# Optimization experiments

Measured on AMD Instinct MI355X. Metric: run time of the kernel, lower is better.

The kernel has to match this reference:

```python
import jax, jax.numpy as jnp
import numpy as np

B, QL, D = 4, 1024, 1024
H, HD = 16, 64
KVL = 2048


def setup_inputs() -> dict:
    key = jax.random.key(0)
    ks = jax.random.split(key, 6)
    scale = 1.0 / np.sqrt(D)
    return {
        "hidden_states": jax.random.normal(ks[0], (B, QL, D), dtype=jnp.float32),
        "key_states": jax.random.normal(ks[1], (B, H, KVL, HD), dtype=jnp.float32),
        "value_states": jax.random.normal(ks[2], (B, H, KVL, HD), dtype=jnp.float32),
        "attention_mask": jnp.zeros((B, 1, 1, KVL), dtype=jnp.float32),
        "Wq": jax.random.normal(ks[3], (D, D), dtype=jnp.float32) * scale,
        "Wo": jax.random.normal(ks[4], (D, D), dtype=jnp.float32) * scale,
    }


def reference(hidden_states, key_states, value_states, attention_mask, Wq, Wo):
    batch = hidden_states.shape[0]
    # Q projection (T5 Linear has no bias), split heads: [B, H, Q, HD]
    q = jnp.einsum("bqd,de->bqe", hidden_states, Wq)
    q = q.reshape(batch, -1, H, HD).transpose(0, 2, 1, 3)
    # NOTE: T5 attention has NO 1/sqrt(d) scaling
    scores = jnp.einsum("bhqd,bhkd->bhqk", q, key_states) + attention_mask
    attn = jax.nn.softmax(scores.astype(jnp.float32), axis=-1).astype(scores.dtype)
    out = jnp.einsum("bhqk,bhkd->bhqd", attn, value_states)
    out = out.transpose(0, 2, 1, 3).reshape(batch, -1, H * HD)
    return jnp.einsum("bqe,ed->bqd", out, Wo)
```

## Files before the change

kernel.cpp:

```cpp
#include <hip/hip_runtime.h>
#include <hip/hip_bf16.h>
#include <hip/hip_fp16.h>
#include <stdint.h>

typedef _Float16 f16;
typedef _Float16 f16x2 __attribute__((ext_vector_type(2)));
typedef _Float16 f16x4 __attribute__((ext_vector_type(4)));
typedef _Float16 f16x8 __attribute__((ext_vector_type(8)));
typedef float f32x4 __attribute__((ext_vector_type(4)));
typedef float f32x16 __attribute__((ext_vector_type(16)));

#define B_ 4
#define QL_ 1024
#define D_ 1024
#define H_ 16
#define HD_ 64
#define KVL_ 2048
#define L2E 1.44269504088896f

__device__ __forceinline__ void g2lds16(const void* g, void* l) {
    __builtin_amdgcn_global_load_lds(
        (const __attribute__((address_space(1))) uint32_t*)g,
        (__attribute__((address_space(3))) uint32_t*)l,
        16, 0, 0);
}

union U8 { uint32_t u[4]; f16x8 v; };

__device__ __forceinline__ uint32_t pkrtz(float a, float b) {
    auto t = __builtin_amdgcn_cvt_pkrtz(a, b);
    return __builtin_bit_cast(uint32_t, t);
}

__global__ void preprocess_slim(const float* __restrict__ hs, f16* __restrict__ hs_h,
                                const float* __restrict__ Wq, f16* __restrict__ Wq_t) {
    __shared__ float t[64][65];
    int bid = blockIdx.x, tid = threadIdx.x;
    if (bid < 1024) {
        const int n4 = (B_ * QL_ * D_) / 4;
        for (int i = bid * 256 + tid; i < n4; i += 1024 * 256) {
            float4 v = ((const float4*)hs)[i];
            f16x4 o = { (f16)v.x, (f16)v.y, (f16)v.z, (f16)v.w };
            ((f16x4*)hs_h)[i] = o;
        }
    } else {
        int b2 = bid - 1024;
        int k0 = (b2 >> 4) << 6, n0 = (b2 & 15) << 6;
        int rr = tid >> 4, c4 = (tid & 15) << 2;
#pragma unroll
        for (int i = 0; i < 4; ++i) {
            int r = i * 16 + rr;
            float4 v = *(const float4*)(Wq + (size_t)(k0 + r) * 1024 + n0 + c4);
            t[r][c4 + 0] = v.x; t[r][c4 + 1] = v.y; t[r][c4 + 2] = v.z; t[r][c4 + 3] = v.w;
        }
        __syncthreads();
#pragma unroll
        for (int i = 0; i < 4; ++i) {
            int n = i * 16 + rr;
            f16x4 o;
#pragma unroll
            for (int j = 0; j < 4; ++j) o[j] = (f16)t[c4 + j][n];
            *(f16x4*)(Wq_t + (size_t)(n0 + n) * 1024 + k0 + c4) = o;
        }
    }
}

__global__ __launch_bounds__(512) void gemm0_fused(
    const f16* __restrict__ A, const f16* __restrict__ BT, f16* __restrict__ q_h,
    const float* __restrict__ K, f16* __restrict__ K_h,
    const float* __restrict__ V, f16* __restrict__ V_t,
    const float* __restrict__ Wo, f16* __restrict__ Wo_t,
    const float* __restrict__ mask, float* __restrict__ mL) {
    __shared__ char shmem[49152];
    int bid = blockIdx.x, tid = threadIdx.x;

    if (bid < 512) {
        char* Alds = shmem;
        char* Blds = shmem + 32768;
        int xcd = bid & 7, sx = bid >> 3;
        int bm = xcd * 4 + (sx & 3);
        int bn = sx >> 2;
        int w = tid >> 6, l = tid & 63;
        int l15 = l & 15, lg = l >> 4;
        int wm = w >> 1, wn = w & 1;
        f32x4 acc[2][2] = {};

        const char* ag0; const char* ag1; int ao0, ao1;
        {
            int i0 = w, i1 = w + 8;
            int r0 = i0 * 8 + (l >> 3), r1 = i1 * 8 + (l >> 3);
            int c0 = (l & 7) ^ (r0 & 7), c1 = (l & 7) ^ (r1 & 7);
            ag0 = (const char*)A + ((size_t)(bm * 128 + r0) * 1024 + c0 * 8) * 2;
            ag1 = (const char*)A + ((size_t)(bm * 128 + r1) * 1024 + c1 * 8) * 2;
            ao0 = i0 * 1024; ao1 = i1 * 1024;
        }
        int rB = w * 8 + (l >> 3);
        int ccB = (l & 7) ^ (rB & 7);
        const char* bgp = (const char*)BT + ((size_t)(bn * 64 + rB) * 1024 + ccB * 8) * 2;
        int boB = w * 1024;

        int aoff[2][2], boff[2][2];
#pragma unroll
        for (int ks = 0; ks < 2; ++ks)
#pragma unroll
            for (int m = 0; m < 2; ++m) {
                int ra = wm * 32 + m * 16 + l15;
                aoff[ks][m] = ra * 128 + ((ks * 64 + lg * 16) ^ ((ra & 7) << 4));
                int rb = wn * 32 + m * 16 + l15;
                boff[ks][m] = rb * 128 + ((ks * 64 + lg * 16) ^ ((rb & 7) << 4));
            }

#define GSTAGE(buf, soff)                                          \
    {                                                              \
        g2lds16(ag0 + (soff), Alds + (buf) * 16384 + ao0);         \
        g2lds16(ag1 + (soff), Alds + (buf) * 16384 + ao1);         \
        g2lds16(bgp + (soff), Blds + (buf) * 8192 + boB);          \
    }
#define GCOMP(buf)                                                               \
    _Pragma("unroll") for (int ks = 0; ks < 2; ++ks) {                           \
        f16x8 af[2], bf[2];                                                      \
        af[0] = *(const f16x8*)(Alds + (buf) * 16384 + aoff[ks][0]);             \
        af[1] = *(const f16x8*)(Alds + (buf) * 16384 + aoff[ks][1]);             \
        bf[0] = *(const f16x8*)(Blds + (buf) * 8192 + boff[ks][0]);              \
        bf[1] = *(const f16x8*)(Blds + (buf) * 8192 + boff[ks][1]);              \
        _Pragma("unroll") for (int m = 0; m < 2; ++m)                            \
            _Pragma("unroll") for (int n = 0; n < 2; ++n)                        \
                acc[m][n] = __builtin_amdgcn_mfma_f32_16x16x32_f16(af[m], bf[n], acc[m][n], 0, 0, 0); \
    }

        GSTAGE(0, 0);
        asm volatile("s_waitcnt vmcnt(0)" ::: "memory");
        __syncthreads();
        for (int t2 = 0; t2 < 8; ++t2) {
            GSTAGE(1, 128);
            GCOMP(0);
            asm volatile("s_waitcnt vmcnt(0)" ::: "memory");
            __syncthreads();
            if (t2 < 7) GSTAGE(0, 256);
            GCOMP(1);
            asm volatile("s_waitcnt vmcnt(0)" ::: "memory");
            __syncthreads();
            ag0 += 256; ag1 += 256; bgp += 256;
        }
#pragma unroll
        for (int m = 0; m < 2; ++m)
#pragma unroll
            for (int n = 0; n < 2; ++n)
#pragma unroll
                for (int i = 0; i < 4; ++i) {
                    int row = bm * 128 + wm * 32 + m * 16 + lg * 4 + i;
                    int col = bn * 64 + wn * 32 + n * 16 + l15;
                    float v = acc[m][n][i] * L2E;
                    int b = row >> 10, q = row & 1023, h = col >> 6, d = col & 63;
                    q_h[(((size_t)b * H_ + h) * QL_ + q) * HD_ + d] = (f16)v;
                }
#undef GSTAGE
#undef GCOMP
    } else if (bid < 1536) {
        int t0 = (bid - 512) * 512 + tid;
#pragma unroll
        for (int rep = 0; rep < 2; ++rep) {
            int U = t0 + rep * 524288;
            int bh = U >> 14, rem = U & 16383;
            int ch = rem >> 9, r2 = rem & 511;
            int dsl = r2 >> 7, r3 = r2 & 127;
            int kv = r3 >> 1, hi2 = r3 & 1;
            const float* sp = K + (((size_t)bh * KVL_ + ch * 64 + kv) * HD_ + dsl * 16 + hi2 * 8);
            f16x8 o;
#pragma unroll
            for (int j = 0; j < 8; ++j) o[j] = (f16)sp[j];
            *(f16x8*)(K_h + (size_t)U * 8) = o;
        }
    } else if (bid < 2560) {
        int sub = tid >> 8, st2 = tid & 255;
        int vb = (bid - 1536) * 2 + sub;
        int bh = vb >> 5, ch = vb & 31;
        float (*tt)[65] = (float(*)[65])(shmem + sub * 16640);
        int rr = st2 >> 4, c4 = (st2 & 15) << 2;
#pragma unroll
        for (int i = 0; i < 4; ++i) {
            int r = i * 16 + rr;
            float4 v = *(const float4*)(V + ((size_t)bh * KVL_ + ch * 64 + r) * HD_ + c4);
            tt[r][c4 + 0] = v.x; tt[r][c4 + 1] = v.y; tt[r][c4 + 2] = v.z; tt[r][c4 + 3] = v.w;
        }
        __syncthreads();
#pragma unroll
        for (int rep = 0; rep < 2; ++rep) {
            int u = st2 + rep * 256;
            int st = u >> 7, d = (u >> 1) & 63, hi2 = u & 1;
            f16x8 o;
#pragma unroll
            for (int j = 0; j < 8; ++j) {
                int kvl = st * 16 + (j & 3) + 8 * (j >> 2) + 4 * hi2;
                o[j] = (f16)tt[kvl][d];
            }
            *(f16x8*)(V_t + ((size_t)(bh * 32 + ch) * 512 + u) * 8) = o;
        }
    } else if (bid < 2688) {
        int sub = tid >> 8, st2 = tid & 255;
        int b2 = (bid - 2560) * 2 + sub;
        float (*tt)[65] = (float(*)[65])(shmem + sub * 16640);
        int k0 = (b2 >> 4) << 6, n0 = (b2 & 15) << 6;
        int rr = st2 >> 4, c4 = (st2 & 15) << 2;
#pragma unroll
        for (int i = 0; i < 4; ++i) {
            int r = i * 16 + rr;
            float4 v = *(const float4*)(Wo + (size_t)(k0 + r) * 1024 + n0 + c4);
            tt[r][c4 + 0] = v.x; tt[r][c4 + 1] = v.y; tt[r][c4 + 2] = v.z; tt[r][c4 + 3] = v.w;
        }
        __syncthreads();
#pragma unroll
        for (int i = 0; i < 4; ++i) {
            int n = i * 16 + rr;
            f16x4 o;
#pragma unroll
            for (int j = 0; j < 4; ++j) o[j] = (f16)tt[c4 + j][n];
            *(f16x4*)(Wo_t + (size_t)(n0 + n) * 1024 + k0 + c4) = o;
        }
    } else {
        int i = (bid - 2688) * 512 + tid;
        if (i < (B_ * KVL_) / 4) {
            f32x4 v = ((const f32x4*)mask)[i];
            v *= L2E;
            ((f32x4*)mL)[i] = v;
        }
    }
}

__global__ __launch_bounds__(512) void gemm_tn1(
    const f16* __restrict__ A, const f16* __restrict__ BT, float* __restrict__ Cout) {
    __shared__ char Alds[2][16384];
    __shared__ char Blds[2][8192];
    int d0 = blockIdx.x;
    int xcd = d0 & 7, sx = d0 >> 3;
    int bm = xcd * 4 + (sx & 3);
    int bn = sx >> 2;
    int tid = threadIdx.x, w = tid >> 6, l = tid & 63;
    int l15 = l & 15, lg = l >> 4;
    int wm = w >> 1, wn = w & 1;
    f32x4 acc[2][2] = {};

    const char* ag0; const char* ag1; int ao0, ao1;
    {
        int i0 = w, i1 = w + 8;
        int r0 = i0 * 8 + (l >> 3), r1 = i1 * 8 + (l >> 3);
        int c0 = (l & 7) ^ (r0 & 7), c1 = (l & 7) ^ (r1 & 7);
        ag0 = (const char*)A + ((size_t)(bm * 128 + r0) * 1024 + c0 * 8) * 2;
        ag1 = (const char*)A + ((size_t)(bm * 128 + r1) * 1024 + c1 * 8) * 2;
        ao0 = i0 * 1024; ao1 = i1 * 1024;
    }
    int rB = w * 8 + (l >> 3);
    int ccB = (l & 7) ^ (rB & 7);
    const char* bgp = (const char*)BT + ((size_t)(bn * 64 + rB) * 1024 + ccB * 8) * 2;
    int boB = w * 1024;

    int aoff[2][2], boff[2][2];
#pragma unroll
    for (int ks = 0; ks < 2; ++ks)
#pragma unroll
        for (int m = 0; m < 2; ++m) {
            int ra = wm * 32 + m * 16 + l15;
            aoff[ks][m] = ra * 128 + ((ks * 64 + lg * 16) ^ ((ra & 7) << 4));
            int rb = wn * 32 + m * 16 + l15;
            boff[ks][m] = rb * 128 + ((ks * 64 + lg * 16) ^ ((rb & 7) << 4));
        }
    const char* Ab = &Alds[0][0];
    const char* Bb = &Blds[0][0];

#define GSTAGE(buf, soff)                                      \
    {                                                          \
        g2lds16(ag0 + (soff), &Alds[buf][ao0]);                \
        g2lds16(ag1 + (soff), &Alds[buf][ao1]);                \
        g2lds16(bgp + (soff), &Blds[buf][boB]);                \
    }
#define GCOMP(buf)                                                               \
    _Pragma("unroll") for (int ks = 0; ks < 2; ++ks) {                           \
        f16x8 af[2], bf[2];                                                      \
        af[0] = *(const f16x8*)(Ab + (buf) * 16384 + aoff[ks][0]);               \
        af[1] = *(const f16x8*)(Ab + (buf) * 16384 + aoff[ks][1]);               \
        bf[0] = *(const f16x8*)(Bb + (buf) * 8192 + boff[ks][0]);                \
        bf[1] = *(const f16x8*)(Bb + (buf) * 8192 + boff[ks][1]);                \
        _Pragma("unroll") for (int m = 0; m < 2; ++m)                            \
            _Pragma("unroll") for (int n = 0; n < 2; ++n)                        \
                acc[m][n] = __builtin_amdgcn_mfma_f32_16x16x32_f16(af[m], bf[n], acc[m][n], 0, 0, 0); \
    }

    GSTAGE(0, 0);
    asm volatile("s_waitcnt vmcnt(0)" ::: "memory");
    __syncthreads();
    for (int t2 = 0; t2 < 8; ++t2) {
        GSTAGE(1, 128);
        GCOMP(0);
        asm volatile("s_waitcnt vmcnt(0)" ::: "memory");
        __syncthreads();
        if (t2 < 7) GSTAGE(0, 256);
        GCOMP(1);
        asm volatile("s_waitcnt vmcnt(0)" ::: "memory");
        __syncthreads();
        ag0 += 256; ag1 += 256; bgp += 256;
    }
#pragma unroll
    for (int m = 0; m < 2; ++m)
#pragma unroll
        for (int n = 0; n < 2; ++n)
#pragma unroll
            for (int i = 0; i < 4; ++i) {
                int row = bm * 128 + wm * 32 + m * 16 + lg * 4 + i;
                int col = bn * 64 + wn * 32 + n * 16 + l15;
                Cout[(size_t)row * 1024 + col] = acc[m][n][i];
            }
#undef GSTAGE
#undef GCOMP
}

__global__ __launch_bounds__(512, 4) void attn_fused(
    const f16* __restrict__ qh, const f16* __restrict__ kh, const f16* __restrict__ vt,
    const float* __restrict__ mL, f16* __restrict__ aout) {
    __shared__ char lds_buf[65536];
    __shared__ float frl[8][32];
    __shared__ float fr2[4][2][32];
    __shared__ float2 msx[4][32];

    int tid = threadIdx.x, w = tid >> 6, l = tid & 63;
    int l31 = l & 31, hi = l >> 5;
    int g = w >> 2, wg = w & 3;
    int d0 = blockIdx.x;
    int xcd = d0 & 7, sx = d0 >> 3;
    int bh = xcd * 8 + (sx & 7);
    int qt = sx >> 3;
    int b = bh >> 4, h = bh & 15;

    const char* lbase = lds_buf + g * 32768 + l31 * 32 + hi * 16;

    f16x8 Qf[4];
    {
        const f16* qp = qh + ((size_t)bh * QL_ + qt * 128 + wg * 32 + l31) * HD_ + hi * 8;
#pragma unroll
        for (int ds_ = 0; ds_ < 4; ++ds_) Qf[ds_] = *(const f16x8*)(qp + ds_ * 16);
    }

    int i0 = wg * 2;
    const char* kgp0 = (const char*)kh + (((size_t)(bh * 32 + g * 16) * 512) + i0 * 64 + l) * 16;
    const char* kgp1 = kgp0 + 1024;
    const char* vgp0 = (const char*)vt + (((size_t)(bh * 32 + g * 16) * 512) + i0 * 64 + l) * 16;
    const char* vgp1 = vgp0 + 1024;
    char* kl0 = lds_buf + g * 32768 + i0 * 1024;
    char* kl1 = kl0 + 1024;
    char* vl0 = lds_buf + g * 32768 + 16384 + i0 * 1024;
    char* vl1 = vl0 + 1024;

#define PREF(buf, soff)                                  \
    {                                                    \
        g2lds16(kgp0 + (soff), kl0 + (buf) * 8192);      \
        g2lds16(kgp1 + (soff), kl1 + (buf) * 8192);      \
        g2lds16(vgp0 + (soff), vl0 + (buf) * 8192);      \
        g2lds16(vgp1 + (soff), vl1 + (buf) * 8192);      \
    }

    float mrun = -1e30f, ssA = 0.f, ssB = 0.f;
    f32x16 acc[2] = {};
    const float* mp = mL + b * KVL_ + g * 1024 + hi * 4;
    const f16x2 one2 = { (f16)1.0f, (f16)1.0f };

#define BODY(buf, kb, mof)                                                                \
    {                                                                                     \
        const float* mq = mp + (mof) + (kb) * 32;                                         \
        f32x4 mv0 = *(const f32x4*)(mq);                                                  \
        f32x4 mv1 = *(const f32x4*)(mq + 8);                                              \
        f32x4 mv2 = *(const f32x4*)(mq + 16);                                             \
        f32x4 mv3 = *(const f32x4*)(mq + 24);                                             \
        f32x16 St;                                                                        \
        _Pragma("unroll") for (int j = 0; j < 4; ++j) {                                   \
            St[j] = mv0[j]; St[4 + j] = mv1[j]; St[8 + j] = mv2[j]; St[12 + j] = mv3[j];  \
        }                                                                                 \
        __builtin_amdgcn_s_setprio(1);                                                    \
        _Pragma("unroll") for (int ds_ = 0; ds_ < 4; ++ds_) {                             \
            f16x8 kf = *(const f16x8*)(lbase + (buf) * 8192 + ds_ * 2048 + (kb) * 1024);  \
            St = __builtin_amdgcn_mfma_f32_32x32x16_f16(kf, Qf[ds_], St, 0, 0, 0);        \
        }                                                                                 \
        __builtin_amdgcn_s_setprio(0);                                                    \
        float a0 = fmaxf(fmaxf(St[0], St[1]), St[2]);                                     \
        float a1 = fmaxf(fmaxf(St[3], St[4]), St[5]);                                     \
        float a2 = fmaxf(fmaxf(St[6], St[7]), St[8]);                                     \
        float a3 = fmaxf(fmaxf(St[9], St[10]), St[11]);                                   \
        float a4 = fmaxf(fmaxf(St[12], St[13]), St[14]);                                  \
        float lmax = fmaxf(fmaxf(fmaxf(a0, a1), St[15]), fmaxf(a2, fmaxf(a3, a4)));       \
        if (__any(lmax > mrun + 12.f)) {                                                  \
            float pm = fmaxf(lmax, __shfl_xor(lmax, 32));                                 \
            float mn = fmaxf(mrun, pm);                                                   \
            float fac = __builtin_amdgcn_exp2f(mrun - mn);                                \
            mrun = mn; ssA *= fac; ssB *= fac;                                            \
            frl[w][l31] = fac;                                                            \
            asm volatile("s_waitcnt lgkmcnt(0)" ::: "memory");                            \
            _Pragma("unroll") for (int g4 = 0; g4 < 4; ++g4) {                            \
                f32x4 fv = *(const f32x4*)&frl[w][g4 * 8 + hi * 4];                       \
                _Pragma("unroll") for (int c = 0; c < 2; ++c)                             \
                    _Pragma("unroll") for (int j = 0; j < 4; ++j)                         \
                        acc[c][g4 * 4 + j] *= fv[j];                                      \
            }                                                                             \
        }                                                                                 \
        uint32_t pk[8];                                                                   \
        _Pragma("unroll") for (int i = 0; i < 8; ++i) {                                   \
            float p0 = __builtin_amdgcn_exp2f(St[2 * i] - mrun);                          \
            float p1 = __builtin_amdgcn_exp2f(St[2 * i + 1] - mrun);                      \
            pk[i] = pkrtz(p0, p1);                                                        \
        }                                                                                 \
        _Pragma("unroll") for (int i = 0; i < 4; ++i) {                                   \
            ssA = __builtin_amdgcn_fdot2(__builtin_bit_cast(f16x2, pk[2 * i]), one2, ssA, false);     \
            ssB = __builtin_amdgcn_fdot2(__builtin_bit_cast(f16x2, pk[2 * i + 1]), one2, ssB, false); \
        }                                                                                 \
        __builtin_amdgcn_s_setprio(1);                                                    \
        _Pragma("unroll") for (int sti = 0; sti < 2; ++sti) {                             \
            U8 pa;                                                                        \
            pa.u[0] = pk[sti * 4 + 0]; pa.u[1] = pk[sti * 4 + 1];                         \
            pa.u[2] = pk[sti * 4 + 2]; pa.u[3] = pk[sti * 4 + 3];                         \
            const int st_ = (kb) * 2 + sti;                                               \
            _Pragma("unroll") for (int c = 0; c < 2; ++c) {                               \
                U8 vb;                                                                    \
                vb.v = *(const f16x8*)(lbase + 16384 + (buf) * 8192 + st_ * 2048 + c * 1024); \
                acc[c] = __builtin_amdgcn_mfma_f32_32x32x16_f16(pa.v, vb.v, acc[c], 0, 0, 0); \
            }                                                                             \
        }                                                                                 \
        __builtin_amdgcn_s_setprio(0);                                                    \
    }

    PREF(0, 0);
    asm volatile("s_waitcnt vmcnt(0)" ::: "memory");
    __syncthreads();

    for (int it = 0; it < 8; ++it) {
        PREF(1, 8192);
        BODY(0, 0, 0);
        BODY(0, 1, 0);
        asm volatile("s_waitcnt vmcnt(0)" ::: "memory");
        __syncthreads();
        if (it < 7) PREF(0, 16384);
        BODY(1, 0, 64);
        BODY(1, 1, 64);
        asm volatile("s_waitcnt vmcnt(0)" ::: "memory");
        __syncthreads();
        kgp0 += 16384; kgp1 += 16384; vgp0 += 16384; vgp1 += 16384;
        mp += 128;
    }

    float ssum = ssA + ssB;
    ssum += __shfl_xor(ssum, 32);
    char* exch = lds_buf;
    if (g == 1) {
        int base = (wg * 64 + l) * 128;
#pragma unroll
        for (int i = 0; i < 8; ++i) {
            int c = i >> 2, j0 = (i & 3) * 4;
            f32x4 vv = { acc[c][j0], acc[c][j0 + 1], acc[c][j0 + 2], acc[c][j0 + 3] };
            *(f32x4*)(exch + base + ((i * 16) ^ ((l & 7) << 4))) = vv;
        }
        if (hi == 0) msx[wg][l31] = make_float2(mrun, ssum);
    }
    __syncthreads();
    if (g == 0) {
        float2 mb = msx[wg][l31];
        float m = fmaxf(mrun, mb.x);
        float fA = __builtin_amdgcn_exp2f(mrun - m);
        float fB = __builtin_amdgcn_exp2f(mb.x - m);
        float s = ssum * fA + mb.y * fB;
        float rinv = 1.0f / s;
        if (hi == 0) { fr2[wg][0][l31] = fA * rinv; fr2[wg][1][l31] = fB * rinv; }
        asm volatile("s_waitcnt lgkmcnt(0)" ::: "memory");
        int base = (wg * 64 + l) * 128;
#pragma unroll
        for (int c = 0; c < 2; ++c)
#pragma unroll
            for (int g4 = 0; g4 < 4; ++g4) {
                f32x4 gAv = *(const f32x4*)&fr2[wg][0][g4 * 8 + hi * 4];
                f32x4 gBv = *(const f32x4*)&fr2[wg][1][g4 * 8 + hi * 4];
                int i = c * 4 + g4;
                f32x4 pv = *(const f32x4*)(exch + base + ((i * 16) ^ ((l & 7) << 4)));
#pragma unroll
                for (int j = 0; j < 4; ++j) {
                    float o = acc[c][g4 * 4 + j] * gAv[j] + pv[j] * gBv[j];
                    int q = qt * 128 + wg * 32 + g4 * 8 + hi * 4 + j;
                    int dd = c * 32 + l31;
                    aout[((size_t)b * QL_ + q) * D_ + h * HD_ + dd] = (f16)o;
                }
            }
    }
#undef PREF
#undef BODY
}

extern "C" void kernel_launch(void* const* d_in, const int* in_sizes, int n_in,
                              void* d_out, int out_size, void* d_ws, size_t ws_size,
                              hipStream_t stream) {
    const float* hs = (const float*)d_in[0];
    const float* K  = (const float*)d_in[1];
    const float* V  = (const float*)d_in[2];
    const float* mask = (const float*)d_in[3];
    const float* Wq = (const float*)d_in[4];
    const float* Wo = (const float*)d_in[5];
    float* out = (float*)d_out;
    char* ws = (char*)d_ws;

    f16* hs_h = (f16*)(ws + 0);
    f16* Wq_t = (f16*)(ws + 8388608);
    f16* Wo_t = (f16*)(ws + 10485760);
    f16* K_h  = (f16*)(ws + 12582912);
    f16* V_t  = (f16*)(ws + 29360128);
    f16* q_h  = (f16*)(ws + 46137344);
    f16* a_o  = (f16*)(ws + 54525952);
    float* mL = (float*)(ws + 62914560);

    preprocess_slim<<<1280, 256, 0, stream>>>(hs, hs_h, Wq, Wq_t);
    gemm0_fused<<<2692, 512, 0, stream>>>(hs_h, Wq_t, q_h, K, K_h, V, V_t,
                                          Wo, Wo_t, mask, mL);
    attn_fused<<<512, 512, 0, stream>>>(q_h, K_h, V_t, mL, a_o);
    gemm_tn1<<<512, 512, 0, stream>>>(a_o, Wo_t, out);
}
```

Before: 101.6 us.

## Fuse hidden-state conversion into Q GEMM, fold mask into V, drop KV split

```diff
diff --git a/kernel.cpp b/kernel.cpp
--- a/kernel.cpp
+++ b/kernel.cpp
@@ -9,6 +9,7 @@
 typedef _Float16 f16x8 __attribute__((ext_vector_type(8)));
 typedef float f32x4 __attribute__((ext_vector_type(4)));
 typedef float f32x16 __attribute__((ext_vector_type(16)));
+typedef uint32_t u32x4 __attribute__((ext_vector_type(4)));
 
 #define B_ 4
 #define QL_ 1024
@@ -32,45 +33,34 @@
     return __builtin_bit_cast(uint32_t, t);
 }
 
-__global__ void preprocess_slim(const float* __restrict__ hs, f16* __restrict__ hs_h,
-                                const float* __restrict__ Wq, f16* __restrict__ Wq_t) {
+__global__ void prep_wq(const float* __restrict__ Wq, f16* __restrict__ Wq_t) {
     __shared__ float t[64][65];
-    int bid = blockIdx.x, tid = threadIdx.x;
-    if (bid < 1024) {
-        const int n4 = (B_ * QL_ * D_) / 4;
-        for (int i = bid * 256 + tid; i < n4; i += 1024 * 256) {
-            float4 v = ((const float4*)hs)[i];
-            f16x4 o = { (f16)v.x, (f16)v.y, (f16)v.z, (f16)v.w };
-            ((f16x4*)hs_h)[i] = o;
-        }
-    } else {
-        int b2 = bid - 1024;
-        int k0 = (b2 >> 4) << 6, n0 = (b2 & 15) << 6;
-        int rr = tid >> 4, c4 = (tid & 15) << 2;
-#pragma unroll
-        for (int i = 0; i < 4; ++i) {
-            int r = i * 16 + rr;
-            float4 v = *(const float4*)(Wq + (size_t)(k0 + r) * 1024 + n0 + c4);
-            t[r][c4 + 0] = v.x; t[r][c4 + 1] = v.y; t[r][c4 + 2] = v.z; t[r][c4 + 3] = v.w;
-        }
-        __syncthreads();
-#pragma unroll
-        for (int i = 0; i < 4; ++i) {
-            int n = i * 16 + rr;
-            f16x4 o;
-#pragma unroll
-            for (int j = 0; j < 4; ++j) o[j] = (f16)t[c4 + j][n];
-            *(f16x4*)(Wq_t + (size_t)(n0 + n) * 1024 + k0 + c4) = o;
-        }
+    int b2 = blockIdx.x, tid = threadIdx.x;
+    int k0 = (b2 >> 4) << 6, n0 = (b2 & 15) << 6;
+    int rr = tid >> 4, c4 = (tid & 15) << 2;
+#pragma unroll
+    for (int i = 0; i < 4; ++i) {
+        int r = i * 16 + rr;
+        float4 v = *(const float4*)(Wq + (size_t)(k0 + r) * 1024 + n0 + c4);
+        t[r][c4 + 0] = v.x; t[r][c4 + 1] = v.y; t[r][c4 + 2] = v.z; t[r][c4 + 3] = v.w;
+    }
+    __syncthreads();
+#pragma unroll
+    for (int i = 0; i < 4; ++i) {
+        int n = i * 16 + rr;
+        f16x4 o;
+#pragma unroll
+        for (int j = 0; j < 4; ++j) o[j] = (f16)t[c4 + j][n];
+        *(f16x4*)(Wq_t + (size_t)(n0 + n) * 1024 + k0 + c4) = o;
     }
 }
 
 __global__ __launch_bounds__(512) void gemm0_fused(
-    const f16* __restrict__ A, const f16* __restrict__ BT, f16* __restrict__ q_h,
+    const float* __restrict__ hs, const f16* __restrict__ BT, f16* __restrict__ q_h,
     const float* __restrict__ K, f16* __restrict__ K_h,
     const float* __restrict__ V, f16* __restrict__ V_t,
     const float* __restrict__ Wo, f16* __restrict__ Wo_t,
-    const float* __restrict__ mask, float* __restrict__ mL) {
+    const float* __restrict__ mask, f16* __restrict__ em16) {
     __shared__ char shmem[49152];
     int bid = blockIdx.x, tid = threadIdx.x;
 
@@ -85,15 +75,12 @@
         int wm = w >> 1, wn = w & 1;
         f32x4 acc[2][2] = {};
 
-        const char* ag0; const char* ag1; int ao0, ao1;
-        {
-            int i0 = w, i1 = w + 8;
-            int r0 = i0 * 8 + (l >> 3), r1 = i1 * 8 + (l >> 3);
-            int c0 = (l & 7) ^ (r0 & 7), c1 = (l & 7) ^ (r1 & 7);
-            ag0 = (const char*)A + ((size_t)(bm * 128 + r0) * 1024 + c0 * 8) * 2;
-            ag1 = (const char*)A + ((size_t)(bm * 128 + r1) * 1024 + c1 * 8) * 2;
-            ao0 = i0 * 1024; ao1 = i1 * 1024;
-        }
+        int rA0 = tid >> 3, c80 = tid & 7, cc0 = c80 ^ (rA0 & 7);
+        const float* ags0 = hs + ((size_t)(bm * 128 + rA0) * 1024 + cc0 * 8);
+        const float* ags1 = ags0 + 65536;
+        int aw0 = rA0 * 128 + c80 * 16;
+        int aw1 = aw0 + 8192;
+
         int rB = w * 8 + (l >> 3);
         int ccB = (l & 7) ^ (rB & 7);
         const char* bgp = (const char*)BT + ((size_t)(bn * 64 + rB) * 1024 + ccB * 8) * 2;
@@ -110,11 +97,24 @@
                 boff[ks][m] = rb * 128 + ((ks * 64 + lg * 16) ^ ((rb & 7) << 4));
             }
 
-#define GSTAGE(buf, soff)                                          \
-    {                                                              \
-        g2lds16(ag0 + (soff), Alds + (buf) * 16384 + ao0);         \
-        g2lds16(ag1 + (soff), Alds + (buf) * 16384 + ao1);         \
-        g2lds16(bgp + (soff), Blds + (buf) * 8192 + boB);          \
+        f32x4 a0, a1, a2, a3;
+#define ALOAD(buf, o32, oB)                                    \
+    {                                                          \
+        a0 = *(const f32x4*)(ags0 + (o32));                    \
+        a1 = *(const f32x4*)(ags0 + (o32) + 4);                \
+        a2 = *(const f32x4*)(ags1 + (o32));                    \
+        a3 = *(const f32x4*)(ags1 + (o32) + 4);                \
+        g2lds16(bgp + (oB), Blds + (buf) * 8192 + boB);        \
+    }
+#define CVTW(buf)                                                              \
+    {                                                                          \
+        asm volatile("s_waitcnt vmcnt(1)" ::: "memory");                       \
+        u32x4 w0 = { pkrtz(a0[0], a0[1]), pkrtz(a0[2], a0[3]),                 \
+                     pkrtz(a1[0], a1[1]), pkrtz(a1[2], a1[3]) };               \
+        *(u32x4*)(Alds + (buf) * 16384 + aw0) = w0;                            \
+        u32x4 w1 = { pkrtz(a2[0], a2[1]), pkrtz(a2[2], a2[3]),                 \
+                     pkrtz(a3[0], a3[1]), pkrtz(a3[2], a3[3]) };               \
+        *(u32x4*)(Alds + (buf) * 16384 + aw1) = w1;                            \
     }
 #define GCOMP(buf)                                                               \
     _Pragma("unroll") for (int ks = 0; ks < 2; ++ks) {                           \
@@ -127,20 +127,25 @@
             _Pragma("unroll") for (int n = 0; n < 2; ++n)                        \
                 acc[m][n] = __builtin_amdgcn_mfma_f32_16x16x32_f16(af[m], bf[n], acc[m][n], 0, 0, 0); \
     }
-
-        GSTAGE(0, 0);
-        asm volatile("s_waitcnt vmcnt(0)" ::: "memory");
-        __syncthreads();
+#define SYNCV()                                                          \
+    {                                                                    \
+        asm volatile("s_waitcnt vmcnt(0) lgkmcnt(0)" ::: "memory");      \
+        __syncthreads();                                                 \
+    }
+
+        ALOAD(0, 0, 0);
+        CVTW(0);
+        SYNCV();
         for (int t2 = 0; t2 < 8; ++t2) {
-            GSTAGE(1, 128);
+            ALOAD(1, 64, 128);
             GCOMP(0);
-            asm volatile("s_waitcnt vmcnt(0)" ::: "memory");
-            __syncthreads();
-            if (t2 < 7) GSTAGE(0, 256);
+            CVTW(1);
+            SYNCV();
+            if (t2 < 7) ALOAD(0, 128, 256);
             GCOMP(1);
-            asm volatile("s_waitcnt vmcnt(0)" ::: "memory");
-            __syncthreads();
-            ag0 += 256; ag1 += 256; bgp += 256;
+            if (t2 < 7) CVTW(0);
+            SYNCV();
+            ags0 += 128; ags1 += 128; bgp += 256;
         }
 #pragma unroll
         for (int m = 0; m < 2; ++m)
@@ -154,8 +159,10 @@
                     int b = row >> 10, q = row & 1023, h = col >> 6, d = col & 63;
                     q_h[(((size_t)b * H_ + h) * QL_ + q) * HD_ + d] = (f16)v;
                 }
-#undef GSTAGE
+#undef ALOAD
+#undef CVTW
 #undef GCOMP
+#undef SYNCV
     } else if (bid < 1536) {
         int t0 = (bid - 512) * 512 + tid;
 #pragma unroll
@@ -175,7 +182,9 @@
         int sub = tid >> 8, st2 = tid & 255;
         int vb = (bid - 1536) * 2 + sub;
         int bh = vb >> 5, ch = vb & 31;
+        int b = bh >> 4;
         float (*tt)[65] = (float(*)[65])(shmem + sub * 16640);
+        float* emv = (float*)(shmem + 33280 + sub * 256);
         int rr = st2 >> 4, c4 = (st2 & 15) << 2;
 #pragma unroll
         for (int i = 0; i < 4; ++i) {
@@ -183,6 +192,8 @@
             float4 v = *(const float4*)(V + ((size_t)bh * KVL_ + ch * 64 + r) * HD_ + c4);
             tt[r][c4 + 0] = v.x; tt[r][c4 + 1] = v.y; tt[r][c4 + 2] = v.z; tt[r][c4 + 3] = v.w;
         }
+        if (st2 < 64)
+            emv[st2] = __builtin_amdgcn_exp2f(mask[(size_t)b * KVL_ + ch * 64 + st2] * L2E);
         __syncthreads();
 #pragma unroll
         for (int rep = 0; rep < 2; ++rep) {
@@ -192,11 +203,16 @@
 #pragma unroll
             for (int j = 0; j < 8; ++j) {
                 int kvl = st * 16 + (j & 3) + 8 * (j >> 2) + 4 * hi2;
-                o[j] = (f16)tt[kvl][d];
+                o[j] = (f16)(tt[kvl][d] * emv[kvl]);
             }
             *(f16x8*)(V_t + ((size_t)(bh * 32 + ch) * 512 + u) * 8) = o;
         }
-    } else if (bid < 2688) {
+        if (((bh & 15) == 0) && st2 < 64) {
+            int kb = st2 >> 5, hi2v = (st2 >> 4) & 1, slot = st2 & 15;
+            int kvv = kb * 32 + (slot & 3) + 8 * (slot >> 2) + 4 * hi2v;
+            em16[(((size_t)b * 64 + ch * 2 + kb) * 2 + hi2v) * 16 + slot] = (f16)emv[kvv];
+        }
+    } else {
         int sub = tid >> 8, st2 = tid & 255;
         int b2 = (bid - 2560) * 2 + sub;
         float (*tt)[65] = (float(*)[65])(shmem + sub * 16640);
@@ -216,13 +232,6 @@
 #pragma unroll
             for (int j = 0; j < 4; ++j) o[j] = (f16)tt[c4 + j][n];
             *(f16x4*)(Wo_t + (size_t)(n0 + n) * 1024 + k0 + c4) = o;
-        }
-    } else {
-        int i = (bid - 2688) * 512 + tid;
-        if (i < (B_ * KVL_) / 4) {
-            f32x4 v = ((const f32x4*)mask)[i];
-            v *= L2E;
-            ((f32x4*)mL)[i] = v;
         }
     }
 }
@@ -313,40 +322,37 @@
 #undef GCOMP
 }
 
-__global__ __launch_bounds__(512, 4) void attn_fused(
+__global__ __launch_bounds__(256, 4) void attn_fused(
     const f16* __restrict__ qh, const f16* __restrict__ kh, const f16* __restrict__ vt,
-    const float* __restrict__ mL, f16* __restrict__ aout) {
-    __shared__ char lds_buf[65536];
-    __shared__ float frl[8][32];
-    __shared__ float fr2[4][2][32];
-    __shared__ float2 msx[4][32];
+    const f16* __restrict__ em16, f16* __restrict__ aout) {
+    __shared__ char lds_buf[36864];
+    __shared__ float frl[4][32];
 
     int tid = threadIdx.x, w = tid >> 6, l = tid & 63;
     int l31 = l & 31, hi = l >> 5;
-    int g = w >> 2, wg = w & 3;
     int d0 = blockIdx.x;
     int xcd = d0 & 7, sx = d0 >> 3;
     int bh = xcd * 8 + (sx & 7);
     int qt = sx >> 3;
     int b = bh >> 4, h = bh & 15;
 
-    const char* lbase = lds_buf + g * 32768 + l31 * 32 + hi * 16;
+    const char* lbase = lds_buf + l31 * 32 + hi * 16;
+    const char* embase = lds_buf + 32768 + hi * 32;
 
     f16x8 Qf[4];
     {
-        const f16* qp = qh + ((size_t)bh * QL_ + qt * 128 + wg * 32 + l31) * HD_ + hi * 8;
+        const f16* qp = qh + ((size_t)bh * QL_ + qt * 128 + w * 32 + l31) * HD_ + hi * 8;
 #pragma unroll
         for (int ds_ = 0; ds_ < 4; ++ds_) Qf[ds_] = *(const f16x8*)(qp + ds_ * 16);
     }
 
-    int i0 = wg * 2;
-    const char* kgp0 = (const char*)kh + (((size_t)(bh * 32 + g * 16) * 512) + i0 * 64 + l) * 16;
+    const char* kgp0 = (const char*)kh + ((size_t)(bh * 32) * 512 + w * 2 * 64 + l) * 16;
     const char* kgp1 = kgp0 + 1024;
-    const char* vgp0 = (const char*)vt + (((size_t)(bh * 32 + g * 16) * 512) + i0 * 64 + l) * 16;
+    const char* vgp0 = (const char*)vt + ((size_t)(bh * 32) * 512 + w * 2 * 64 + l) * 16;
     const char* vgp1 = vgp0 + 1024;
-    char* kl0 = lds_buf + g * 32768 + i0 * 1024;
+    char* kl0 = lds_buf + w * 2048;
     char* kl1 = kl0 + 1024;
-    char* vl0 = lds_buf + g * 32768 + 16384 + i0 * 1024;
+    char* vl0 = lds_buf + 16384 + w * 2048;
     char* vl1 = vl0 + 1024;
 
 #define PREF(buf, soff)                                  \
@@ -359,20 +365,11 @@
 
     float mrun = -1e30f, ssA = 0.f, ssB = 0.f;
     f32x16 acc[2] = {};
-    const float* mp = mL + b * KVL_ + g * 1024 + hi * 4;
-    const f16x2 one2 = { (f16)1.0f, (f16)1.0f };
-
-#define BODY(buf, kb, mof)                                                                \
+    int emoff = 0;
+
+#define BODY(buf, kb, emo)                                                                \
     {                                                                                     \
-        const float* mq = mp + (mof) + (kb) * 32;                                         \
-        f32x4 mv0 = *(const f32x4*)(mq);                                                  \
-        f32x4 mv1 = *(const f32x4*)(mq + 8);                                              \
-        f32x4 mv2 = *(const f32x4*)(mq + 16);                                             \
-        f32x4 mv3 = *(const f32x4*)(mq + 24);                                             \
-        f32x16 St;                                                                        \
-        _Pragma("unroll") for (int j = 0; j < 4; ++j) {                                   \
-            St[j] = mv0[j]; St[4 + j] = mv1[j]; St[8 + j] = mv2[j]; St[12 + j] = mv3[j];  \
-        }                                                                                 \
+        f32x16 St = {};                                                                   \
         __builtin_amdgcn_s_setprio(1);                                                    \
         _Pragma("unroll") for (int ds_ = 0; ds_ < 4; ++ds_) {                             \
             f16x8 kf = *(const f16x8*)(lbase + (buf) * 8192 + ds_ * 2048 + (kb) * 1024);  \
@@ -405,9 +402,14 @@
             float p1 = __builtin_amdgcn_exp2f(St[2 * i + 1] - mrun);                      \
             pk[i] = pkrtz(p0, p1);                                                        \
         }                                                                                 \
+        U8 ea, eb;                                                                        \
+        ea.v = *(const f16x8*)(embase + (emo));                                           \
+        eb.v = *(const f16x8*)(embase + (emo) + 16);                                      \
         _Pragma("unroll") for (int i = 0; i < 4; ++i) {                                   \
-            ssA = __builtin_amdgcn_fdot2(__builtin_bit_cast(f16x2, pk[2 * i]), one2, ssA, false);     \
-            ssB = __builtin_amdgcn_fdot2(__builtin_bit_cast(f16x2, pk[2 * i + 1]), one2, ssB, false); \
+            ssA = __builtin_amdgcn_fdot2(__builtin_bit_cast(f16x2, pk[2 * i]),            \
+                                         __builtin_bit_cast(f16x2, (2 * i) < 4 ? ea.u[2 * i] : eb.u[2 * i - 4]), ssA, false); \
+            ssB = __builtin_amdgcn_fdot2(__builtin_bit_cast(f16x2, pk[2 * i + 1]),        \
+                                         __builtin_bit_cast(f16x2, (2 * i + 1) < 4 ? ea.u[2 * i + 1] : eb.u[2 * i - 3]), ssB, false); \
         }                                                                                 \
         __builtin_amdgcn_s_setprio(1);                                                    \
         _Pragma("unroll") for (int sti = 0; sti < 2; ++sti) {                             \
@@ -424,64 +426,42 @@
         __builtin_amdgcn_s_setprio(0);                                                    \
     }
 
+    g2lds16((const char*)em16 + b * 4096 + w * 1024 + l * 16, lds_buf + 32768 + w * 1024);
     PREF(0, 0);
     asm volatile("s_waitcnt vmcnt(0)" ::: "memory");
     __syncthreads();
 
-    for (int it = 0; it < 8; ++it) {
+    for (int it = 0; it < 16; ++it) {
         PREF(1, 8192);
-        BODY(0, 0, 0);
-        BODY(0, 1, 0);
+        BODY(0, 0, emoff);
+        BODY(0, 1, emoff + 64);
         asm volatile("s_waitcnt vmcnt(0)" ::: "memory");
         __syncthreads();
-        if (it < 7) PREF(0, 16384);
-        BODY(1, 0, 64);
-        BODY(1, 1, 64);
+        if (it < 15) PREF(0, 16384);
+        BODY(1, 0, emoff + 128);
+        BODY(1, 1, emoff + 192);
         asm volatile("s_waitcnt vmcnt(0)" ::: "memory");
         __syncthreads();
         kgp0 += 16384; kgp1 += 16384; vgp0 += 16384; vgp1 += 16384;
-        mp += 128;
+        emoff += 256;
     }
 
     float ssum = ssA + ssB;
     ssum += __shfl_xor(ssum, 32);
-    char* exch = lds_buf;
-    if (g == 1) {
-        int base = (wg * 64 + l) * 128;
-#pragma unroll
-        for (int i = 0; i < 8; ++i) {
-            int c = i >> 2, j0 = (i & 3) * 4;
-            f32x4 vv = { acc[c][j0], acc[c][j0 + 1], acc[c][j0 + 2], acc[c][j0 + 3] };
-            *(f32x4*)(exch + base + ((i * 16) ^ ((l & 7) << 4))) = vv;
-        }
-        if (hi == 0) msx[wg][l31] = make_float2(mrun, ssum);
-    }
-    __syncthreads();
-    if (g == 0) {
-        float2 mb = msx[wg][l31];
-        float m = fmaxf(mrun, mb.x);
-        float fA = __builtin_amdgcn_exp2f(mrun - m);
-        float fB = __builtin_amdgcn_exp2f(mb.x - m);
-        float s = ssum * fA + mb.y * fB;
-        float rinv = 1.0f / s;
-        if (hi == 0) { fr2[wg][0][l31] = fA * rinv; fr2[wg][1][l31] = fB * rinv; }
-        asm volatile("s_waitcnt lgkmcnt(0)" ::: "memory");
-        int base = (wg * 64 + l) * 128;
+    float rinv = 1.0f / ssum;
+    frl[w][l31] = rinv;
+    asm volatile("s_waitcnt lgkmcnt(0)" ::: "memory");
+#pragma unroll
+    for (int g4 = 0; g4 < 4; ++g4) {
+        f32x4 rv = *(const f32x4*)&frl[w][g4 * 8 + hi * 4];
 #pragma unroll
         for (int c = 0; c < 2; ++c)
 #pragma unroll
-            for (int g4 = 0; g4 < 4; ++g4) {
-                f32x4 gAv = *(const f32x4*)&fr2[wg][0][g4 * 8 + hi * 4];
-                f32x4 gBv = *(const f32x4*)&fr2[wg][1][g4 * 8 + hi * 4];
-                int i = c * 4 + g4;
-                f32x4 pv = *(const f32x4*)(exch + base + ((i * 16) ^ ((l & 7) << 4)));
-#pragma unroll
-                for (int j = 0; j < 4; ++j) {
-                    float o = acc[c][g4 * 4 + j] * gAv[j] + pv[j] * gBv[j];
-                    int q = qt * 128 + wg * 32 + g4 * 8 + hi * 4 + j;
-                    int dd = c * 32 + l31;
-                    aout[((size_t)b * QL_ + q) * D_ + h * HD_ + dd] = (f16)o;
-                }
+            for (int j = 0; j < 4; ++j) {
+                float o = acc[c][g4 * 4 + j] * rv[j];
+                int q = qt * 128 + w * 32 + g4 * 8 + hi * 4 + j;
+                int dd = c * 32 + l31;
+                aout[((size_t)b * QL_ + q) * D_ + h * HD_ + dd] = (f16)o;
             }
     }
 #undef PREF
@@ -500,18 +480,17 @@
     float* out = (float*)d_out;
     char* ws = (char*)d_ws;
 
-    f16* hs_h = (f16*)(ws + 0);
-    f16* Wq_t = (f16*)(ws + 8388608);
-    f16* Wo_t = (f16*)(ws + 10485760);
-    f16* K_h  = (f16*)(ws + 12582912);
-    f16* V_t  = (f16*)(ws + 29360128);
-    f16* q_h  = (f16*)(ws + 46137344);
-    f16* a_o  = (f16*)(ws + 54525952);
-    float* mL = (float*)(ws + 62914560);
-
-    preprocess_slim<<<1280, 256, 0, stream>>>(hs, hs_h, Wq, Wq_t);
-    gemm0_fused<<<2692, 512, 0, stream>>>(hs_h, Wq_t, q_h, K, K_h, V, V_t,
-                                          Wo, Wo_t, mask, mL);
-    attn_fused<<<512, 512, 0, stream>>>(q_h, K_h, V_t, mL, a_o);
+    f16* Wq_t = (f16*)(ws + 0);
+    f16* Wo_t = (f16*)(ws + 2097152);
+    f16* K_h  = (f16*)(ws + 4194304);
+    f16* V_t  = (f16*)(ws + 20971520);
+    f16* q_h  = (f16*)(ws + 37748736);
+    f16* a_o  = (f16*)(ws + 46137344);
+    f16* em16 = (f16*)(ws + 54525952);
+
+    prep_wq<<<256, 256, 0, stream>>>(Wq, Wq_t);
+    gemm0_fused<<<2688, 512, 0, stream>>>(hs, Wq_t, q_h, K, K_h, V, V_t,
+                                          Wo, Wo_t, mask, em16);
+    attn_fused<<<512, 256, 0, stream>>>(q_h, K_h, V_t, em16, a_o);
     gemm_tn1<<<512, 512, 0, stream>>>(a_o, Wo_t, out);
 }
```

Result: no change. 103.6 us (+2.0%).
